# Optimization experiments

Hardware: AMD Instinct MI355X
Metric: run time of the kernel (lower is better)

## Reference

```python
import jax, jax.numpy as jnp
import numpy as np

Q = 4096  # num_quantizing
E = 256   # quantizing_dim


def setup_inputs() -> dict:
    key = jax.random.key(0)
    kx, kw = jax.random.split(key)
    x = jax.random.normal(kx, (16, 2048, E), dtype=jnp.float32)
    # nn.init.normal_(weight, mean=0.0, std=0.001)
    weight = 0.001 * jax.random.normal(kw, (Q, E), dtype=jnp.float32)
    return {"x": x, "weight": weight}


def reference(x, weight):
    # x: (*, E), weight: (Q, E)
    input_shape = x.shape
    xf = x.reshape(-1, weight.shape[1])  # (N, E)
    # Squared L2 distance via norm expansion (same argmin as sum(delta^2)):
    x2 = jnp.sum(xf * xf, axis=1, keepdims=True)          # (N, 1)
    w2 = jnp.sum(weight * weight, axis=1)                  # (Q,)
    dist = x2 - 2.0 * (xf @ weight.T) + w2                 # (N, Q)
    q_idx = jnp.argmin(dist, axis=1)                       # (N,)
    q_data = weight[q_idx]                                 # (N, E)
    return q_data.reshape(input_shape), q_idx.reshape(input_shape[:-1])
```

## Files before the change

### kernel.cpp

```cpp
#include <hip/hip_runtime.h>
#include <cfloat>
#include <climits>

constexpr int E  = 256;
constexpr int Qn = 4096;
constexpr float WSCALE = 4096.0f;


typedef _Float16 half8  __attribute__((ext_vector_type(8)));
typedef _Float16 half4v __attribute__((ext_vector_type(4)));
typedef float    f32x16 __attribute__((ext_vector_type(16)));

#define GAS __attribute__((address_space(1)))
#define LAS __attribute__((address_space(3)))

#define NEG_INF __int_as_float(0xFF800000)

__device__ inline bool lexlt(float a, int ai, float b, int bi) {
    return a < b || (a == b && ai < bi);
}

__global__ __launch_bounds__(256) void prep_kernel(
    const float* __restrict__ x, const float* __restrict__ w,
    _Float16* __restrict__ A16, _Float16* __restrict__ B16,
    float* __restrict__ w2, int nxblocks)
{
    int blk  = blockIdx.x;
    int sub  = threadIdx.x >> 6;
    int lane = threadIdx.x & 63;
    bool isX = blk < nxblocks;
    int row  = (isX ? blk : blk - nxblocks) * 4 + sub;

    const float* src = isX ? x : w;
    float4 v = *(const float4*)(src + (size_t)row * E + lane * 4);

    if (!isX) {
        float s = v.x * v.x + v.y * v.y + v.z * v.z + v.w * v.w;
        #pragma unroll
        for (int off = 32; off; off >>= 1) s += __shfl_xor(s, off);
        if (lane == 0) w2[row] = s;
    }

    float sc = isX ? 1.0f : WSCALE;
    half4v h = { (_Float16)(v.x * sc), (_Float16)(v.y * sc),
                 (_Float16)(v.z * sc), (_Float16)(v.w * sc) };
    _Float16* dst16 = (isX ? A16 : B16) + (size_t)row * 256;
    *(half4v*)(dst16 + lane * 4) = h;
}

__device__ inline void ins4max(float K[4], float k) {
    #pragma unroll
    for (int t = 0; t < 4; ++t) {
        float mx = fmaxf(K[t], k);
        k = fminf(K[t], k);
        K[t] = mx;
    }
}

union SmemU {
    _Float16 buf[2][4][128][64];
    float2 mergeS[128 * 16];
};

__global__ __launch_bounds__(512, 2) void vq_mfma_kernel(
    const _Float16* __restrict__ A16,
    const _Float16* __restrict__ B16,
    float4* __restrict__ top4)
{
    __shared__ SmemU sm;

    const int tid  = threadIdx.x;
    const int wv   = tid >> 6;
    const int lane = tid & 63;
    const int l31  = lane & 31;
    const int lh   = lane >> 5;
    const int rb   = blockIdx.x;

    const int cwg = wv & 3;
    const int rg  = wv >> 2;

    const _Float16* Ab16 = A16 + (size_t)rb * 128 * 256;

    auto stage128 = [&](const _Float16* src, int bi) {
        #pragma unroll
        for (int kt = 0; kt < 4; ++kt)
            #pragma unroll
            for (int i = 0; i < 2; ++i) {
                int row  = i * 64 + wv * 8 + (lane >> 3);
                int gchk = (lane & 7) ^ (row & 7);
                const _Float16* g = src + (size_t)row * 256 + kt * 64 + gchk * 8;
                __builtin_amdgcn_global_load_lds((const GAS void*)g,
                    (LAS void*)(&sm.buf[bi][kt][i * 64 + wv * 8][0]), 16, 0, 0);
            }
    };

    stage128(Ab16, 0);
    stage128(B16, 1);
    __syncthreads();

    half8 xf[2][4][4];
    #pragma unroll
    for (int n = 0; n < 2; ++n)
        #pragma unroll
        for (int kt = 0; kt < 4; ++kt)
            #pragma unroll
            for (int s = 0; s < 4; ++s) {
                int xr = rg * 64 + n * 32 + l31;
                int kc = 2 * s + lh;
                xf[n][kt][s] = *(const half8*)(&sm.buf[0][kt][0][0]
                                + xr * 64 + ((kc ^ (xr & 7)) << 3));
            }
    __syncthreads();

    float t1[2][4], t2[2][4];
    #pragma unroll
    for (int n = 0; n < 2; ++n)
        #pragma unroll
        for (int q = 0; q < 4; ++q) { t1[n][q] = NEG_INF; t2[n][q] = NEG_INF; }

    const int fr = cwg * 32 + l31;
    const int frsw = fr & 7;

    #pragma unroll
    for (int q = 0; q < 4; ++q) {
        for (int tt = 0; tt < 8; ++tt) {
            const int t  = q * 8 + tt;
            const int bi = (t + 1) & 1;

            if (t + 1 < 32)
                stage128(B16 + (size_t)(t + 1) * 128 * 256, t & 1);

            const _Float16* Wb = &sm.buf[bi][0][0][0];

            f32x16 acc0 = {}, acc1 = {};
            __builtin_amdgcn_s_setprio(1);
            #pragma unroll
            for (int kt = 0; kt < 4; ++kt)
                #pragma unroll
                for (int s = 0; s < 4; ++s) {
                    int kc = 2 * s + lh;
                    half8 wf = *(const half8*)(Wb + kt * 8192
                                  + fr * 64 + ((kc ^ frsw) << 3));
                    acc0 = __builtin_amdgcn_mfma_f32_32x32x16_f16(
                               wf, xf[0][kt][s], acc0, 0, 0, 0);
                    acc1 = __builtin_amdgcn_mfma_f32_32x32x16_f16(
                               wf, xf[1][kt][s], acc1, 0, 0, 0);
                }
            __builtin_amdgcn_s_setprio(0);

            #pragma unroll
            for (int r = 0; r < 16; ++r) {
                int crow = (r & 3) + 8 * (r >> 2) + 4 * lh;
                int qg   = t * 128 + cwg * 32 + crow;
                float pk0 = __int_as_float(
                    (__float_as_int(acc0[r]) & 0xFFFFF000) | qg);
                t2[0][q] = __builtin_amdgcn_fmed3f(t1[0][q], t2[0][q], pk0);
                t1[0][q] = fmaxf(t1[0][q], pk0);
                float pk1 = __int_as_float(
                    (__float_as_int(acc1[r]) & 0xFFFFF000) | qg);
                t2[1][q] = __builtin_amdgcn_fmed3f(t1[1][q], t2[1][q], pk1);
                t1[1][q] = fmaxf(t1[1][q], pk1);
            }

            __syncthreads();
        }
    }

    #pragma unroll
    for (int n = 0; n < 2; ++n)
        #pragma unroll
        for (int q = 0; q < 4; ++q) {
            float o1 = __shfl_xor(t1[n][q], 32);
            float o2 = __shfl_xor(t2[n][q], 32);
            float m1 = fmaxf(t1[n][q], o1);
            float m2 = __builtin_amdgcn_fmed3f(t1[n][q], o1,
                                               fmaxf(t2[n][q], o2));
            t1[n][q] = m1; t2[n][q] = m2;
        }

    if (lh == 0) {
        #pragma unroll
        for (int n = 0; n < 2; ++n) {
            int row = rg * 64 + n * 32 + l31;
            #pragma unroll
            for (int q = 0; q < 4; ++q)
                sm.mergeS[row * 16 + cwg * 4 + q] =
                    make_float2(t1[n][q], t2[n][q]);
        }
    }
    __syncthreads();

    if (tid < 128) {
        float K[4] = { NEG_INF, NEG_INF, NEG_INF, NEG_INF };
        #pragma unroll
        for (int sl = 0; sl < 16; ++sl) {
            float2 a = sm.mergeS[tid * 16 + sl];
            ins4max(K, a.x);
            ins4max(K, a.y);
        }
        top4[(size_t)rb * 128 + tid] = make_float4(K[0], K[1], K[2], K[3]);
    }
}

__global__ __launch_bounds__(256) void finalize_kernel(
    const float4* __restrict__ top4, const float* __restrict__ x,
    const float* __restrict__ w, const float* __restrict__ w2,
    float* __restrict__ qdata, float* __restrict__ qidx)
{
    int row  = blockIdx.x * 4 + (threadIdx.x >> 6);
    int lane = threadIdx.x & 63;

    float4 c4 = top4[row];
    int chosen[4] = { __float_as_int(c4.x) & 0xFFF,
                      __float_as_int(c4.y) & 0xFFF,
                      __float_as_int(c4.z) & 0xFFF,
                      __float_as_int(c4.w) & 0xFFF };

    float4 xv = *(const float4*)(x + (size_t)row * E + lane * 4);
    float s2 = xv.x * xv.x + xv.y * xv.y + xv.z * xv.z + xv.w * xv.w;
    float d[4];
    #pragma unroll
    for (int j = 0; j < 4; ++j) {
        float4 wv = *(const float4*)(w + (size_t)chosen[j] * E + lane * 4);
        d[j] = xv.x * wv.x + xv.y * wv.y + xv.z * wv.z + xv.w * wv.w;
    }
    #pragma unroll
    for (int off = 32; off; off >>= 1) {
        s2 += __shfl_xor(s2, off);
        #pragma unroll
        for (int j = 0; j < 4; ++j) d[j] += __shfl_xor(d[j], off);
    }

    float bs = FLT_MAX; int win = INT_MAX;
    #pragma unroll
    for (int j = 0; j < 4; ++j) {
        float s = (s2 - 2.0f * d[j]) + w2[chosen[j]];
        if (lexlt(s, chosen[j], bs, win)) { bs = s; win = chosen[j]; }
    }

    if (lane == 0) qidx[row] = (float)win;
    *(float4*)(qdata + (size_t)row * E + lane * 4) =
        *(const float4*)(w + (size_t)win * E + lane * 4);
}

constexpr int FBM = 64, FBN = 128, FBK = 64, FPAD = 4, FTH = 256;

__global__ __launch_bounds__(64) void row_sumsq_kernel(const float* __restrict__ src,
                                                       float* __restrict__ dst) {
    int row = blockIdx.x, lane = threadIdx.x;
    float4 v = ((const float4*)(src + (size_t)row * E))[lane];
    float s = v.x * v.x + v.y * v.y + v.z * v.z + v.w * v.w;
    #pragma unroll
    for (int off = 32; off > 0; off >>= 1) s += __shfl_down(s, off);
    if (lane == 0) dst[row] = s;
}

__global__ __launch_bounds__(FTH) void vq_fallback_kernel(
    const float* __restrict__ x, const float* __restrict__ w,
    const float* __restrict__ x2, const float* __restrict__ w2,
    float* __restrict__ qdata, float* __restrict__ qidx)
{
    __shared__ float xs[FBM][FBK + FPAD];
    __shared__ float ws[FBN][FBK + FPAD];
    __shared__ float redS[FBM][16];
    __shared__ int   redC[FBM][16];
    __shared__ int   bestC[FBM];

    const int tid = threadIdx.x, tr = tid >> 4, tc = tid & 15;
    const int r0 = blockIdx.x * FBM;
    float best[4]; int bidx[4];
    #pragma unroll
    for (int i = 0; i < 4; ++i) { best[i] = FLT_MAX; bidx[i] = 0x7FFFFFFF; }
    float x2r[4];
    #pragma unroll
    for (int i = 0; i < 4; ++i) x2r[i] = x2[r0 + tr + 16 * i];

    for (int qt = 0; qt < Qn / FBN; ++qt) {
        const int c0 = qt * FBN;
        float acc[4][8];
        #pragma unroll
        for (int i = 0; i < 4; ++i)
            #pragma unroll
            for (int j = 0; j < 8; ++j) acc[i][j] = 0.f;
        for (int kt = 0; kt < E / FBK; ++kt) {
            __syncthreads();
            const int kk = (tid & 15) * 4, rr = tid >> 4;
            #pragma unroll
            for (int m = 0; m < 4; ++m)
                *(float4*)&xs[m * 16 + rr][kk] =
                    *(const float4*)(x + (size_t)(r0 + m * 16 + rr) * E + kt * FBK + kk);
            #pragma unroll
            for (int m = 0; m < 8; ++m)
                *(float4*)&ws[m * 16 + rr][kk] =
                    *(const float4*)(w + (size_t)(c0 + m * 16 + rr) * E + kt * FBK + kk);
            __syncthreads();
            #pragma unroll
            for (int k4 = 0; k4 < FBK / 4; ++k4) {
                float4 a[4], bb[8];
                #pragma unroll
                for (int i = 0; i < 4; ++i) a[i] = *(const float4*)&xs[tr + 16 * i][k4 * 4];
                #pragma unroll
                for (int j = 0; j < 8; ++j) bb[j] = *(const float4*)&ws[tc + 16 * j][k4 * 4];
                #pragma unroll
                for (int i = 0; i < 4; ++i)
                    #pragma unroll
                    for (int j = 0; j < 8; ++j) {
                        acc[i][j] += a[i].x * bb[j].x; acc[i][j] += a[i].y * bb[j].y;
                        acc[i][j] += a[i].z * bb[j].z; acc[i][j] += a[i].w * bb[j].w;
                    }
            }
        }
        #pragma unroll
        for (int i = 0; i < 4; ++i)
            #pragma unroll
            for (int j = 0; j < 8; ++j) {
                int c = c0 + tc + 16 * j;
                float s = (x2r[i] - 2.0f * acc[i][j]) + w2[c];
                if (s < best[i]) { best[i] = s; bidx[i] = c; }
            }
    }
    #pragma unroll
    for (int i = 0; i < 4; ++i) { redS[tr + 16 * i][tc] = best[i]; redC[tr + 16 * i][tc] = bidx[i]; }
    __syncthreads();
    if (tid < FBM) {
        float bs = FLT_MAX; int bc = 0x7FFFFFFF;
        #pragma unroll
        for (int t = 0; t < 16; ++t) {
            float s = redS[tid][t]; int c = redC[tid][t];
            if (s < bs || (s == bs && c < bc)) { bs = s; bc = c; }
        }
        qidx[r0 + tid] = (float)bc; bestC[tid] = bc;
    }
    __syncthreads();
    for (int it = 0; it < FBM / 4; ++it) {
        int row = it * 4 + (tid >> 6), c = bestC[row], kk = (tid & 63) * 4;
        *(float4*)(qdata + (size_t)(r0 + row) * E + kk) = *(const float4*)(w + (size_t)c * E + kk);
    }
}

extern "C" void kernel_launch(void* const* d_in, const int* in_sizes, int n_in,
                              void* d_out, int out_size, void* d_ws, size_t ws_size,
                              hipStream_t stream) {
    const float* x = (const float*)d_in[0];
    const float* w = (const float*)d_in[1];
    const int N = in_sizes[0] / E;

    float* qdata = (float*)d_out;
    float* qidx  = (float*)d_out + (size_t)N * E;

    size_t off = 0;
    auto carve = [&](size_t bytes) { size_t p = off; off += (bytes + 255) & ~(size_t)255; return p; };
    size_t oA16 = carve((size_t)N  * 256 * sizeof(_Float16));
    size_t oB16 = carve((size_t)Qn * 256 * sizeof(_Float16));
    size_t ow2  = carve((size_t)Qn * sizeof(float));
    size_t oT   = carve((size_t)N * sizeof(float4));
    size_t ox2f = carve((size_t)N * sizeof(float));

    if (ws_size >= off && (N % 128) == 0) {
        char* ws = (char*)d_ws;
        _Float16* A16 = (_Float16*)(ws + oA16);
        _Float16* B16 = (_Float16*)(ws + oB16);
        float* w2    = (float*)(ws + ow2);
        float4* top4 = (float4*)(ws + oT);

        prep_kernel<<<N / 4 + Qn / 4, 256, 0, stream>>>(x, w, A16, B16, w2, N / 4);
        vq_mfma_kernel<<<N / 128, 512, 0, stream>>>(A16, B16, top4);
        finalize_kernel<<<N / 4, 256, 0, stream>>>(top4, x, w, w2, qdata, qidx);
    } else {
        float* x2 = (float*)d_ws;
        float* w2 = x2 + N;
        row_sumsq_kernel<<<N, 64, 0, stream>>>(x, x2);
        row_sumsq_kernel<<<Qn, 64, 0, stream>>>(w, w2);
        vq_fallback_kernel<<<N / FBM, FTH, 0, stream>>>(x, w, x2, w2, qdata, qidx);
    }
}
```

Measured before the change: 178.0 us.

## Deepen weight prefetch to 4-slot half-tile pipeline with explicit vmcnt waits

Splits each 128-row weight tile into two K-halves and stages them into a 4-slot LDS ring, prefetching three half-steps ahead. Replaces the per-tile __syncthreads with an explicit s_waitcnt vmcnt plus s_barrier, so several global-to-LDS loads stay in flight while MFMAs run. This is meant to hide global load latency better than the previous double buffer. In exchange there are twice as many barriers per tile, and correctness depends on hand-tuned vmcnt counts.

```diff
diff --git a/kernel.cpp b/kernel.cpp
--- a/kernel.cpp
+++ b/kernel.cpp
@@ -58,9 +58,50 @@
 }
 
 union SmemU {
-    _Float16 buf[2][4][128][64];
+    _Float16 buf[4][2][128][64];
     float2 mergeS[128 * 16];
 };
+
+#define KSTEP(T, VMSTR, Q, H)                                              \
+  {                                                                        \
+    asm volatile("s_waitcnt " VMSTR ::: "memory");                         \
+    __builtin_amdgcn_s_barrier();                                          \
+    asm volatile("" ::: "memory");                                         \
+    const int t_ = (T);                                                    \
+    if (t_ + 3 < 64) stage_t(t_ + 3);                                      \
+    const _Float16* Wb = &sm.buf[t_ & 3][0][0][0];                         \
+    if ((H) == 0) { acc0 = (f32x16){}; acc1 = (f32x16){}; }                \
+    __builtin_amdgcn_s_setprio(1);                                         \
+    _Pragma("unroll")                                                      \
+    for (int ktl = 0; ktl < 2; ++ktl)                                      \
+      _Pragma("unroll")                                                    \
+      for (int s = 0; s < 4; ++s) {                                        \
+        int kc = 2 * s + lh;                                               \
+        half8 wf = *(const half8*)(Wb + ktl * 8192                         \
+                      + fr * 64 + ((kc ^ frsw) << 3));                     \
+        acc0 = __builtin_amdgcn_mfma_f32_32x32x16_f16(                     \
+                   wf, xf[0][2 * (H) + ktl][s], acc0, 0, 0, 0);            \
+        acc1 = __builtin_amdgcn_mfma_f32_32x32x16_f16(                     \
+                   wf, xf[1][2 * (H) + ktl][s], acc1, 0, 0, 0);            \
+      }                                                                    \
+    __builtin_amdgcn_s_setprio(0);                                         \
+    if ((H) == 1) {                                                        \
+      const int ct_ = t_ >> 1;                                             \
+      _Pragma("unroll")                                                    \
+      for (int r = 0; r < 16; ++r) {                                       \
+        int crow = (r & 3) + 8 * (r >> 2) + 4 * lh;                        \
+        int qg   = ct_ * 128 + cwg * 32 + crow;                            \
+        float pk0 = __int_as_float(                                        \
+            (__float_as_int(acc0[r]) & 0xFFFFF000) | qg);                  \
+        t2[0][(Q)] = __builtin_amdgcn_fmed3f(t1[0][(Q)], t2[0][(Q)], pk0); \
+        t1[0][(Q)] = fmaxf(t1[0][(Q)], pk0);                               \
+        float pk1 = __int_as_float(                                        \
+            (__float_as_int(acc1[r]) & 0xFFFFF000) | qg);                  \
+        t2[1][(Q)] = __builtin_amdgcn_fmed3f(t1[1][(Q)], t2[1][(Q)], pk1); \
+        t1[1][(Q)] = fmaxf(t1[1][(Q)], pk1);                               \
+      }                                                                    \
+    }                                                                      \
+  }
 
 __global__ __launch_bounds__(512, 2) void vq_mfma_kernel(
     const _Float16* __restrict__ A16,
@@ -79,23 +120,31 @@
     const int cwg = wv & 3;
     const int rg  = wv >> 2;
 
+    const int srow = lane >> 3;
+    const int schk = lane & 7;
+
     const _Float16* Ab16 = A16 + (size_t)rb * 128 * 256;
 
-    auto stage128 = [&](const _Float16* src, int bi) {
-        #pragma unroll
-        for (int kt = 0; kt < 4; ++kt)
+    auto stage_half = [&](const _Float16* src, int slot, int h) {
+        #pragma unroll
+        for (int ktl = 0; ktl < 2; ++ktl)
             #pragma unroll
             for (int i = 0; i < 2; ++i) {
-                int row  = i * 64 + wv * 8 + (lane >> 3);
-                int gchk = (lane & 7) ^ (row & 7);
-                const _Float16* g = src + (size_t)row * 256 + kt * 64 + gchk * 8;
+                int row  = i * 64 + wv * 8 + srow;
+                int gchk = schk ^ (row & 7);
+                const _Float16* g = src + (size_t)row * 256
+                                    + (2 * h + ktl) * 64 + gchk * 8;
                 __builtin_amdgcn_global_load_lds((const GAS void*)g,
-                    (LAS void*)(&sm.buf[bi][kt][i * 64 + wv * 8][0]), 16, 0, 0);
+                    (LAS void*)(&sm.buf[slot][ktl][i * 64 + wv * 8][0]),
+                    16, 0, 0);
             }
     };
-
-    stage128(Ab16, 0);
-    stage128(B16, 1);
+    auto stage_t = [&](int t) {
+        stage_half(B16 + (size_t)(t >> 1) * 128 * 256, t & 3, t & 1);
+    };
+
+    stage_half(Ab16, 0, 0);
+    stage_half(Ab16, 1, 1);
     __syncthreads();
 
     half8 xf[2][4][4];
@@ -107,64 +156,35 @@
             for (int s = 0; s < 4; ++s) {
                 int xr = rg * 64 + n * 32 + l31;
                 int kc = 2 * s + lh;
-                xf[n][kt][s] = *(const half8*)(&sm.buf[0][kt][0][0]
+                xf[n][kt][s] = *(const half8*)(&sm.buf[kt >> 1][kt & 1][0][0]
                                 + xr * 64 + ((kc ^ (xr & 7)) << 3));
             }
     __syncthreads();
 
+    stage_t(0); stage_t(1); stage_t(2);
+
     float t1[2][4], t2[2][4];
     #pragma unroll
     for (int n = 0; n < 2; ++n)
         #pragma unroll
         for (int q = 0; q < 4; ++q) { t1[n][q] = NEG_INF; t2[n][q] = NEG_INF; }
 
-    const int fr = cwg * 32 + l31;
+    const int fr   = cwg * 32 + l31;
     const int frsw = fr & 7;
 
+    f32x16 acc0, acc1;
+
     #pragma unroll
     for (int q = 0; q < 4; ++q) {
-        for (int tt = 0; tt < 8; ++tt) {
-            const int t  = q * 8 + tt;
-            const int bi = (t + 1) & 1;
-
-            if (t + 1 < 32)
-                stage128(B16 + (size_t)(t + 1) * 128 * 256, t & 1);
-
-            const _Float16* Wb = &sm.buf[bi][0][0][0];
-
-            f32x16 acc0 = {}, acc1 = {};
-            __builtin_amdgcn_s_setprio(1);
-            #pragma unroll
-            for (int kt = 0; kt < 4; ++kt)
-                #pragma unroll
-                for (int s = 0; s < 4; ++s) {
-                    int kc = 2 * s + lh;
-                    half8 wf = *(const half8*)(Wb + kt * 8192
-                                  + fr * 64 + ((kc ^ frsw) << 3));
-                    acc0 = __builtin_amdgcn_mfma_f32_32x32x16_f16(
-                               wf, xf[0][kt][s], acc0, 0, 0, 0);
-                    acc1 = __builtin_amdgcn_mfma_f32_32x32x16_f16(
-                               wf, xf[1][kt][s], acc1, 0, 0, 0);
-                }
-            __builtin_amdgcn_s_setprio(0);
-
-            #pragma unroll
-            for (int r = 0; r < 16; ++r) {
-                int crow = (r & 3) + 8 * (r >> 2) + 4 * lh;
-                int qg   = t * 128 + cwg * 32 + crow;
-                float pk0 = __int_as_float(
-                    (__float_as_int(acc0[r]) & 0xFFFFF000) | qg);
-                t2[0][q] = __builtin_amdgcn_fmed3f(t1[0][q], t2[0][q], pk0);
-                t1[0][q] = fmaxf(t1[0][q], pk0);
-                float pk1 = __int_as_float(
-                    (__float_as_int(acc1[r]) & 0xFFFFF000) | qg);
-                t2[1][q] = __builtin_amdgcn_fmed3f(t1[1][q], t2[1][q], pk1);
-                t1[1][q] = fmaxf(t1[1][q], pk1);
-            }
-
-            __syncthreads();
-        }
-    }
+        const int nct = (q == 3) ? 7 : 8;
+        for (int ctt = 0; ctt < nct; ++ctt) {
+            const int t0 = (q * 8 + ctt) * 2;
+            KSTEP(t0,     "vmcnt(8)", q, 0);
+            KSTEP(t0 + 1, "vmcnt(8)", q, 1);
+        }
+    }
+    KSTEP(62, "vmcnt(4)", 3, 0);
+    KSTEP(63, "vmcnt(0)", 3, 1);
 
     #pragma unroll
     for (int n = 0; n < 2; ++n)
@@ -177,6 +197,8 @@
                                                fmaxf(t2[n][q], o2));
             t1[n][q] = m1; t2[n][q] = m2;
         }
+
+    __syncthreads();
 
     if (lh == 0) {
         #pragma unroll
```

Result: no change. 176.6 us (-0.8%).
